# Kernel tuning notes

Hardware: AMD Instinct MI355X
Metric: run time of the kernel (lower is better)

Reference implementation:

```python
import jax, jax.numpy as jnp
import numpy as np

N_HEAD = 16
D_MODEL = 1024
D_K = 64
D_V = 64
LN_EPS = 1e-5


def setup_inputs() -> dict:
    key = jax.random.key(0)
    ks = jax.random.split(key, 12)
    B, S = 4, 1024
    std_qkv = np.sqrt(2.0 / (D_MODEL + D_K)).astype(np.float32)
    inp = {
        "q": jax.random.normal(ks[0], (B, S, D_MODEL), jnp.float32),
        "k": jax.random.normal(ks[1], (B, S, D_MODEL), jnp.float32),
        "v": jax.random.normal(ks[2], (B, S, D_MODEL), jnp.float32),
        "Wq": jax.random.normal(ks[3], (N_HEAD * D_K, D_MODEL), jnp.float32) * std_qkv,
        "bq": jnp.zeros((N_HEAD * D_K,), jnp.float32),
        "Wk": jax.random.normal(ks[4], (N_HEAD * D_K, D_MODEL), jnp.float32) * std_qkv,
        "bk": jnp.zeros((N_HEAD * D_K,), jnp.float32),
        "Wv": jax.random.normal(ks[5], (N_HEAD * D_K, D_MODEL), jnp.float32) * std_qkv,
        "bv": jnp.zeros((N_HEAD * D_K,), jnp.float32),
        "Wfc": jax.random.normal(ks[6], (D_MODEL, N_HEAD * D_V), jnp.float32) * np.sqrt(2.0 / (D_MODEL + N_HEAD * D_V)).astype(np.float32),
        "bfc": jnp.zeros((D_MODEL,), jnp.float32),
        "gamma": jnp.ones((D_MODEL,), jnp.float32),
        "beta": jnp.zeros((D_MODEL,), jnp.float32),
    }
    return inp


def reference(q, k, v, Wq, bq, Wk, bk, Wv, bv, Wfc, bfc, gamma, beta):
    B, S, D = q.shape
    residual = q
    # projections -> [B, S, H, d] -> [B, H, S, d]
    qh = (q @ Wq.T + bq).reshape(B, S, N_HEAD, D_K).transpose(0, 2, 1, 3)
    kh = (k @ Wk.T + bk).reshape(B, S, N_HEAD, D_K).transpose(0, 2, 1, 3)
    vh = (v @ Wv.T + bv).reshape(B, S, N_HEAD, D_V).transpose(0, 2, 1, 3)
    # NOTE: faithful to source -- no 1/sqrt(d_k) scaling (temperature is None)
    scores = jnp.einsum('bhqd,bhkd->bhqk', qh, kh)  # [B, H, S, S]
    attn = jax.nn.softmax(scores, axis=-1)
    out = jnp.einsum('bhqk,bhkd->bhqd', attn, vh)  # [B, H, S, d_v]
    out = out.transpose(0, 2, 1, 3).reshape(B, S, N_HEAD * D_V)
    out = out @ Wfc.T + bfc  # dropout = identity at eval
    x = out + residual
    mu = jnp.mean(x, axis=-1, keepdims=True)
    var = jnp.var(x, axis=-1, keepdims=True)
    y = (x - mu) * jax.lax.rsqrt(var + LN_EPS) * gamma + beta
    # attn returned in source layout: (n_head*batch, S, S)
    attn_flat = attn.transpose(1, 0, 2, 3).reshape(N_HEAD * B, S, S)
    return (y, attn_flat)
```

## Files before the change

### kernel.cpp

```cpp
#include <hip/hip_runtime.h>
#include <stdint.h>

#define B_ 4
#define S_ 1024
#define D_ 1024
#define H_ 16
#define DK_ 64

typedef unsigned short u16;
typedef unsigned int   u32;
typedef short bf16x8 __attribute__((ext_vector_type(8)));
typedef float f32x4  __attribute__((ext_vector_type(4)));

__device__ __forceinline__ u16 f2bf(float x) {
    u32 u = __float_as_uint(x);
    return (u16)((u + 0x7fffu + ((u >> 16) & 1u)) >> 16);
}
__device__ __forceinline__ float bf2f(u16 h) {
    return __uint_as_float(((u32)h) << 16);
}

template <int OMODE>
__global__ __launch_bounds__(256) void gemm_mfma(const float* __restrict__ A,
                                                 const float* __restrict__ W,
                                                 const float* __restrict__ bias,
                                                 float* __restrict__ Cf,
                                                 u16* __restrict__ Chi,
                                                 u16* __restrict__ Clo,
                                                 int M, int N, int K) {
    __shared__ __align__(16) u16 AhS[128][40];
    __shared__ __align__(16) u16 AlS[128][40];
    __shared__ __align__(16) u16 WhS[128][40];
    __shared__ __align__(16) u16 WlS[128][40];

    const int t    = threadIdx.x;
    const int m0   = blockIdx.y * 128;
    const int n0   = blockIdx.x * 128;
    const int srow = t >> 1;
    const int sk   = (t & 1) * 16;
    const int w    = t >> 6;
    const int lane = t & 63;
    const int wr   = w >> 1, wc = w & 1;
    const int fr   = lane & 15;
    const int kg   = lane >> 4;

    const float* Abase = A + (size_t)(m0 + srow) * K + sk;
    const float* Wbase = W + (size_t)(n0 + srow) * K + sk;

    float4 pa[4], pw[4];
#pragma unroll
    for (int i = 0; i < 4; ++i) {
        pa[i] = *(const float4*)(Abase + i * 4);
        pw[i] = *(const float4*)(Wbase + i * 4);
    }

    f32x4 acc[4][4] = {};

    for (int kc = 0; kc < K; kc += 32) {
        u32 hA[8], lA[8], hW[8], lW[8];
#pragma unroll
        for (int i = 0; i < 4; ++i) {
            float xs[4] = {pa[i].x, pa[i].y, pa[i].z, pa[i].w};
            float ys[4] = {pw[i].x, pw[i].y, pw[i].z, pw[i].w};
#pragma unroll
            for (int j = 0; j < 2; ++j) {
                u16 a0 = f2bf(xs[2 * j]), a1 = f2bf(xs[2 * j + 1]);
                hA[i * 2 + j] = (u32)a0 | ((u32)a1 << 16);
                lA[i * 2 + j] = (u32)f2bf(xs[2 * j] - bf2f(a0)) |
                                ((u32)f2bf(xs[2 * j + 1] - bf2f(a1)) << 16);
                u16 w0 = f2bf(ys[2 * j]), w1 = f2bf(ys[2 * j + 1]);
                hW[i * 2 + j] = (u32)w0 | ((u32)w1 << 16);
                lW[i * 2 + j] = (u32)f2bf(ys[2 * j] - bf2f(w0)) |
                                ((u32)f2bf(ys[2 * j + 1] - bf2f(w1)) << 16);
            }
        }
        *(uint4*)&AhS[srow][sk]     = make_uint4(hA[0], hA[1], hA[2], hA[3]);
        *(uint4*)&AhS[srow][sk + 8] = make_uint4(hA[4], hA[5], hA[6], hA[7]);
        *(uint4*)&AlS[srow][sk]     = make_uint4(lA[0], lA[1], lA[2], lA[3]);
        *(uint4*)&AlS[srow][sk + 8] = make_uint4(lA[4], lA[5], lA[6], lA[7]);
        *(uint4*)&WhS[srow][sk]     = make_uint4(hW[0], hW[1], hW[2], hW[3]);
        *(uint4*)&WhS[srow][sk + 8] = make_uint4(hW[4], hW[5], hW[6], hW[7]);
        *(uint4*)&WlS[srow][sk]     = make_uint4(lW[0], lW[1], lW[2], lW[3]);
        *(uint4*)&WlS[srow][sk + 8] = make_uint4(lW[4], lW[5], lW[6], lW[7]);
        __syncthreads();

        if (kc + 32 < K) {
#pragma unroll
            for (int i = 0; i < 4; ++i) {
                pa[i] = *(const float4*)(Abase + kc + 32 + i * 4);
                pw[i] = *(const float4*)(Wbase + kc + 32 + i * 4);
            }
        }

        bf16x8 fah[4], fal[4], fwh[4], fwl[4];
#pragma unroll
        for (int mt = 0; mt < 4; ++mt) {
            fah[mt] = *(const bf16x8*)&AhS[wr * 64 + mt * 16 + fr][kg * 8];
            fal[mt] = *(const bf16x8*)&AlS[wr * 64 + mt * 16 + fr][kg * 8];
        }
#pragma unroll
        for (int nt = 0; nt < 4; ++nt) {
            fwh[nt] = *(const bf16x8*)&WhS[wc * 64 + nt * 16 + fr][kg * 8];
            fwl[nt] = *(const bf16x8*)&WlS[wc * 64 + nt * 16 + fr][kg * 8];
        }
#pragma unroll
        for (int mt = 0; mt < 4; ++mt)
#pragma unroll
            for (int nt = 0; nt < 4; ++nt) {
                acc[mt][nt] = __builtin_amdgcn_mfma_f32_16x16x32_bf16(
                    fah[mt], fwh[nt], acc[mt][nt], 0, 0, 0);
                acc[mt][nt] = __builtin_amdgcn_mfma_f32_16x16x32_bf16(
                    fah[mt], fwl[nt], acc[mt][nt], 0, 0, 0);
                acc[mt][nt] = __builtin_amdgcn_mfma_f32_16x16x32_bf16(
                    fal[mt], fwh[nt], acc[mt][nt], 0, 0, 0);
            }
        __syncthreads();
    }

#pragma unroll
    for (int nt = 0; nt < 4; ++nt) {
        const int n  = n0 + wc * 64 + nt * 16 + fr;
        const float bn = bias[n];
#pragma unroll
        for (int mt = 0; mt < 4; ++mt) {
#pragma unroll
            for (int r = 0; r < 4; ++r) {
                const int m = m0 + wr * 64 + mt * 16 + kg * 4 + r;
                const float v = acc[mt][nt][r] + bn;
                if (OMODE == 0) {
                    Cf[(size_t)m * N + n] = v;
                } else {
                    const int b = m >> 10, s = m & (S_ - 1);
                    const int h = n >> 6, d = n & 63;
                    const size_t off = (((size_t)b * H_ + h) * S_ + s) * DK_ + d;
                    if (OMODE == 2) {
                        Cf[off] = v;
                    } else {
                        const u16 hh = f2bf(v);
                        Chi[off] = hh;
                        Clo[off] = f2bf(v - bf2f(hh));
                    }
                }
            }
        }
    }
}

__global__ __launch_bounds__(256) void scores_mfma(const u16* __restrict__ Qhi,
                                                   const u16* __restrict__ Qlo,
                                                   const u16* __restrict__ Khi,
                                                   const u16* __restrict__ Klo,
                                                   float* __restrict__ Sc) {
    const int bh = blockIdx.z;
    const int b = bh >> 4, h = bh & 15;
    const u16* Qh_g = Qhi + (size_t)bh * S_ * DK_;
    const u16* Ql_g = Qlo + (size_t)bh * S_ * DK_;
    const u16* Kh_g = Khi + (size_t)bh * S_ * DK_;
    const u16* Kl_g = Klo + (size_t)bh * S_ * DK_;
    float* C = Sc + (size_t)(h * B_ + b) * S_ * S_;

    __shared__ __align__(16) u16 AhS[128][40];
    __shared__ __align__(16) u16 AlS[128][40];
    __shared__ __align__(16) u16 WhS[128][40];
    __shared__ __align__(16) u16 WlS[128][40];

    const int t    = threadIdx.x;
    const int m0   = blockIdx.y * 128;
    const int n0   = blockIdx.x * 128;
    const int srow = t >> 1;
    const int sk   = (t & 1) * 16;
    const int w    = t >> 6;
    const int lane = t & 63;
    const int wr   = w >> 1, wc = w & 1;
    const int fr   = lane & 15;
    const int kg   = lane >> 4;

    f32x4 acc[4][4] = {};

    for (int kc = 0; kc < DK_; kc += 32) {
        {
            const size_t qa = (size_t)(m0 + srow) * DK_ + kc + sk;
            const size_t ka = (size_t)(n0 + srow) * DK_ + kc + sk;
            uint4 q0 = *(const uint4*)(Qh_g + qa);
            uint4 q1 = *(const uint4*)(Qh_g + qa + 8);
            uint4 q2 = *(const uint4*)(Ql_g + qa);
            uint4 q3 = *(const uint4*)(Ql_g + qa + 8);
            uint4 k0 = *(const uint4*)(Kh_g + ka);
            uint4 k1 = *(const uint4*)(Kh_g + ka + 8);
            uint4 k2 = *(const uint4*)(Kl_g + ka);
            uint4 k3 = *(const uint4*)(Kl_g + ka + 8);
            *(uint4*)&AhS[srow][sk]     = q0;
            *(uint4*)&AhS[srow][sk + 8] = q1;
            *(uint4*)&AlS[srow][sk]     = q2;
            *(uint4*)&AlS[srow][sk + 8] = q3;
            *(uint4*)&WhS[srow][sk]     = k0;
            *(uint4*)&WhS[srow][sk + 8] = k1;
            *(uint4*)&WlS[srow][sk]     = k2;
            *(uint4*)&WlS[srow][sk + 8] = k3;
        }
        __syncthreads();

        bf16x8 fah[4], fal[4], fwh[4], fwl[4];
#pragma unroll
        for (int mt = 0; mt < 4; ++mt) {
            fah[mt] = *(const bf16x8*)&AhS[wr * 64 + mt * 16 + fr][kg * 8];
            fal[mt] = *(const bf16x8*)&AlS[wr * 64 + mt * 16 + fr][kg * 8];
        }
#pragma unroll
        for (int nt = 0; nt < 4; ++nt) {
            fwh[nt] = *(const bf16x8*)&WhS[wc * 64 + nt * 16 + fr][kg * 8];
            fwl[nt] = *(const bf16x8*)&WlS[wc * 64 + nt * 16 + fr][kg * 8];
        }
#pragma unroll
        for (int mt = 0; mt < 4; ++mt)
#pragma unroll
            for (int nt = 0; nt < 4; ++nt) {
                acc[mt][nt] = __builtin_amdgcn_mfma_f32_16x16x32_bf16(
                    fah[mt], fwh[nt], acc[mt][nt], 0, 0, 0);
                acc[mt][nt] = __builtin_amdgcn_mfma_f32_16x16x32_bf16(
                    fah[mt], fwl[nt], acc[mt][nt], 0, 0, 0);
                acc[mt][nt] = __builtin_amdgcn_mfma_f32_16x16x32_bf16(
                    fal[mt], fwh[nt], acc[mt][nt], 0, 0, 0);
            }
        __syncthreads();
    }

#pragma unroll
    for (int nt = 0; nt < 4; ++nt) {
        const int j = n0 + wc * 64 + nt * 16 + fr;
#pragma unroll
        for (int mt = 0; mt < 4; ++mt) {
#pragma unroll
            for (int r = 0; r < 4; ++r) {
                const int i = m0 + wr * 64 + mt * 16 + kg * 4 + r;
                C[(size_t)i * S_ + j] = acc[mt][nt][r];
            }
        }
    }
}

__global__ __launch_bounds__(256) void softmax_rows(float* __restrict__ attn) {
    const size_t row = blockIdx.x;
    float* p = attn + row * S_;
    const int t = threadIdx.x;

    float4 v = ((const float4*)p)[t];
    float mx = fmaxf(fmaxf(v.x, v.y), fmaxf(v.z, v.w));
#pragma unroll
    for (int o = 32; o > 0; o >>= 1) mx = fmaxf(mx, __shfl_xor(mx, o, 64));

    __shared__ float red[8];
    const int w = t >> 6;
    if ((t & 63) == 0) red[w] = mx;
    __syncthreads();
    mx = fmaxf(fmaxf(red[0], red[1]), fmaxf(red[2], red[3]));

    float4 e;
    e.x = __expf(v.x - mx);
    e.y = __expf(v.y - mx);
    e.z = __expf(v.z - mx);
    e.w = __expf(v.w - mx);
    float s = e.x + e.y + e.z + e.w;
#pragma unroll
    for (int o = 32; o > 0; o >>= 1) s += __shfl_xor(s, o, 64);
    if ((t & 63) == 0) red[4 + w] = s;
    __syncthreads();
    s = red[4] + red[5] + red[6] + red[7];

    const float inv = 1.0f / s;
    e.x *= inv; e.y *= inv; e.z *= inv; e.w *= inv;
    ((float4*)p)[t] = e;
}

__global__ __launch_bounds__(256) void attn_pv(const float* __restrict__ attn,
                                               const float* __restrict__ Vh,
                                               float* __restrict__ ctx) {
    const int bh = blockIdx.y;
    const int b = bh >> 4, h = bh & 15;
    const int i0 = blockIdx.x * 256;
    const int t  = threadIdx.x;
    const int tm = t >> 3;
    const int tn = t & 7;
    const int srow = t >> 2;
    const int scg  = (t & 3) * 4;
    const int vrow = t >> 4;
    const int vcg  = (t & 15) * 4;

    __shared__ float As[16][260];
    __shared__ float Vs[16][68];

    const float* abase = attn + ((size_t)(h * B_ + b) * S_ + i0) * S_;
    const float* vbase = Vh + (size_t)bh * S_ * DK_;

    const float* Ar0 = abase + (size_t)(srow)       * S_ + scg;
    const float* Ar1 = abase + (size_t)(srow + 64)  * S_ + scg;
    const float* Ar2 = abase + (size_t)(srow + 128) * S_ + scg;
    const float* Ar3 = abase + (size_t)(srow + 192) * S_ + scg;
    const float* Vr  = vbase + (size_t)vrow * DK_ + vcg;

    float4 pa0 = *(const float4*)Ar0;
    float4 pa1 = *(const float4*)Ar1;
    float4 pa2 = *(const float4*)Ar2;
    float4 pa3 = *(const float4*)Ar3;
    float4 pv  = *(const float4*)Vr;

    float acc[8][8] = {};

    for (int kc = 0; kc < S_; kc += 16) {
        As[scg + 0][srow]       = pa0.x;
        As[scg + 1][srow]       = pa0.y;
        As[scg + 2][srow]       = pa0.z;
        As[scg + 3][srow]       = pa0.w;
        As[scg + 0][srow + 64]  = pa1.x;
        As[scg + 1][srow + 64]  = pa1.y;
        As[scg + 2][srow + 64]  = pa1.z;
        As[scg + 3][srow + 64]  = pa1.w;
        As[scg + 0][srow + 128] = pa2.x;
        As[scg + 1][srow + 128] = pa2.y;
        As[scg + 2][srow + 128] = pa2.z;
        As[scg + 3][srow + 128] = pa2.w;
        As[scg + 0][srow + 192] = pa3.x;
        As[scg + 1][srow + 192] = pa3.y;
        As[scg + 2][srow + 192] = pa3.z;
        As[scg + 3][srow + 192] = pa3.w;
        *(float4*)&Vs[vrow][vcg] = pv;
        __syncthreads();
        if (kc + 16 < S_) {
            pa0 = *(const float4*)(Ar0 + kc + 16);
            pa1 = *(const float4*)(Ar1 + kc + 16);
            pa2 = *(const float4*)(Ar2 + kc + 16);
            pa3 = *(const float4*)(Ar3 + kc + 16);
            pv  = *(const float4*)(Vr + (size_t)(kc + 16) * DK_);
        }
#pragma unroll
        for (int kk = 0; kk < 16; ++kk) {
            float4 a0 = *(const float4*)&As[kk][tm * 8];
            float4 a1 = *(const float4*)&As[kk][tm * 8 + 4];
            float4 v0 = *(const float4*)&Vs[kk][tn * 4];
            float4 v1 = *(const float4*)&Vs[kk][32 + tn * 4];
            float av[8] = {a0.x, a0.y, a0.z, a0.w, a1.x, a1.y, a1.z, a1.w};
            float vv[8] = {v0.x, v0.y, v0.z, v0.w, v1.x, v1.y, v1.z, v1.w};
#pragma unroll
            for (int i = 0; i < 8; ++i)
#pragma unroll
                for (int j = 0; j < 8; ++j) acc[i][j] += av[i] * vv[j];
        }
        __syncthreads();
    }

#pragma unroll
    for (int i = 0; i < 8; ++i) {
        const int m = i0 + tm * 8 + i;
        float* crow = ctx + ((size_t)b * S_ + m) * D_ + h * DK_;
        *(float4*)(crow + tn * 4) =
            make_float4(acc[i][0], acc[i][1], acc[i][2], acc[i][3]);
        *(float4*)(crow + 32 + tn * 4) =
            make_float4(acc[i][4], acc[i][5], acc[i][6], acc[i][7]);
    }
}

__global__ __launch_bounds__(256) void ln_kernel(const float* __restrict__ X,
                                                 const float* __restrict__ q,
                                                 const float* __restrict__ gamma,
                                                 const float* __restrict__ beta,
                                                 float* __restrict__ y) {
    const int row = blockIdx.x;
    const int t   = threadIdx.x;
    const size_t base = (size_t)row * D_;

    float4 xv = *(const float4*)(X + base + t * 4);
    float4 qv = *(const float4*)(q + base + t * 4);
    const float x0 = xv.x + qv.x, x1 = xv.y + qv.y;
    const float x2 = xv.z + qv.z, x3 = xv.w + qv.w;

    float sum = x0 + x1 + x2 + x3;
    float sq  = x0 * x0 + x1 * x1 + x2 * x2 + x3 * x3;
#pragma unroll
    for (int o = 32; o > 0; o >>= 1) {
        sum += __shfl_xor(sum, o, 64);
        sq  += __shfl_xor(sq, o, 64);
    }
    __shared__ float red[8];
    const int wv = t >> 6;
    if ((t & 63) == 0) { red[wv] = sum; red[4 + wv] = sq; }
    __syncthreads();
    sum = red[0] + red[1] + red[2] + red[3];
    sq  = red[4] + red[5] + red[6] + red[7];

    const float mu  = sum * (1.0f / 1024.0f);
    const float var = sq * (1.0f / 1024.0f) - mu * mu;
    const float rs  = rsqrtf(var + 1e-5f);

    float4 gv = *(const float4*)(gamma + t * 4);
    float4 bv = *(const float4*)(beta + t * 4);
    float4 o;
    o.x = (x0 - mu) * rs * gv.x + bv.x;
    o.y = (x1 - mu) * rs * gv.y + bv.y;
    o.z = (x2 - mu) * rs * gv.z + bv.z;
    o.w = (x3 - mu) * rs * gv.w + bv.w;
    *(float4*)(y + base + t * 4) = o;
}

extern "C" void kernel_launch(void* const* d_in, const int* in_sizes, int n_in,
                              void* d_out, int out_size, void* d_ws, size_t ws_size,
                              hipStream_t stream) {
    const float* q    = (const float*)d_in[0];
    const float* k    = (const float*)d_in[1];
    const float* v    = (const float*)d_in[2];
    const float* Wq   = (const float*)d_in[3];
    const float* bq   = (const float*)d_in[4];
    const float* Wk   = (const float*)d_in[5];
    const float* bk   = (const float*)d_in[6];
    const float* Wv   = (const float*)d_in[7];
    const float* bv   = (const float*)d_in[8];
    const float* Wfc  = (const float*)d_in[9];
    const float* bfc  = (const float*)d_in[10];
    const float* gamma= (const float*)d_in[11];
    const float* beta = (const float*)d_in[12];

    float* y_out    = (float*)d_out;
    float* attn_out = (float*)d_out + (size_t)B_ * S_ * D_;

    float* ws  = (float*)d_ws;
    float* Vh  = ws;
    u16*  Qhi  = (u16*)(ws + 4194304);
    u16*  Qlo  = (u16*)(ws + 6291456);
    u16*  Khi  = (u16*)(ws + 8388608);
    u16*  Klo  = (u16*)(ws + 10485760);
    float* ctx  = ws + 4194304;
    float* xbuf = ws + 8388608;

    const dim3 gg(8, 32), bb(256);
    gemm_mfma<1><<<gg, bb, 0, stream>>>(q, Wq, bq, nullptr, Qhi, Qlo, 4096, 1024, 1024);
    gemm_mfma<1><<<gg, bb, 0, stream>>>(k, Wk, bk, nullptr, Khi, Klo, 4096, 1024, 1024);
    gemm_mfma<2><<<gg, bb, 0, stream>>>(v, Wv, bv, Vh, nullptr, nullptr, 4096, 1024, 1024);

    scores_mfma<<<dim3(8, 8, 64), bb, 0, stream>>>(Qhi, Qlo, Khi, Klo, attn_out);
    softmax_rows<<<dim3(B_ * H_ * S_), bb, 0, stream>>>(attn_out);

    attn_pv<<<dim3(4, 64), bb, 0, stream>>>(attn_out, Vh, ctx);

    gemm_mfma<0><<<gg, bb, 0, stream>>>(ctx, Wfc, bfc, xbuf, nullptr, nullptr, 4096, 1024, 1024);
    ln_kernel<<<4096, 256, 0, stream>>>(xbuf, q, gamma, beta, y_out);
}
```

Before: 809.8 us.

## Fuse scores, softmax and PV into one MFMA attention kernel with bf16 V/ctx

Replaces the separate scores, softmax and fp32 PV kernels with a single kernel. Each block computes a full 32-row strip of scores with split-bf16 MFMA, does the softmax in registers, writes the attention matrix once, and runs P·V on MFMA from bf16 P and a transposed bf16 V. This removes the write-read-write-read round trips of the 256MB attention matrix and the slow scalar-FMA PV loop. The V projection now emits transposed bf16, and the context feeds the output GEMM as bf16 with no low-part correction terms. This lowers precision for P, V and ctx and keeps 128 fp32 accumulators per thread, which may hurt occupancy.

Result: faster. 694.3 us (-14.3%).

```diff
diff --git a/kernel.cpp b/kernel.cpp
--- a/kernel.cpp
+++ b/kernel.cpp
@@ -20,8 +20,8 @@
     return __uint_as_float(((u32)h) << 16);
 }
 
-template <int OMODE>
-__global__ __launch_bounds__(256) void gemm_mfma(const float* __restrict__ A,
+template <int OMODE, int AMODE>
+__global__ __launch_bounds__(256) void gemm_mfma(const void* __restrict__ Ain,
                                                  const float* __restrict__ W,
                                                  const float* __restrict__ bias,
                                                  float* __restrict__ Cf,
@@ -44,59 +44,92 @@
     const int fr   = lane & 15;
     const int kg   = lane >> 4;
 
-    const float* Abase = A + (size_t)(m0 + srow) * K + sk;
+    const float* Af = (const float*)Ain;
+    const u16*   Ab = (const u16*)Ain;
+
     const float* Wbase = W + (size_t)(n0 + srow) * K + sk;
-
-    float4 pa[4], pw[4];
-#pragma unroll
-    for (int i = 0; i < 4; ++i) {
-        pa[i] = *(const float4*)(Abase + i * 4);
-        pw[i] = *(const float4*)(Wbase + i * 4);
+    float4 pw[4];
+#pragma unroll
+    for (int i = 0; i < 4; ++i) pw[i] = *(const float4*)(Wbase + i * 4);
+
+    float4 pa[4];
+    uint4  ua[2];
+    if constexpr (AMODE == 0) {
+        const float* Abase = Af + (size_t)(m0 + srow) * K + sk;
+#pragma unroll
+        for (int i = 0; i < 4; ++i) pa[i] = *(const float4*)(Abase + i * 4);
+    } else {
+        const u16* Abase = Ab + (size_t)(m0 + srow) * K + sk;
+        ua[0] = *(const uint4*)(Abase);
+        ua[1] = *(const uint4*)(Abase + 8);
     }
 
     f32x4 acc[4][4] = {};
 
     for (int kc = 0; kc < K; kc += 32) {
-        u32 hA[8], lA[8], hW[8], lW[8];
-#pragma unroll
-        for (int i = 0; i < 4; ++i) {
-            float xs[4] = {pa[i].x, pa[i].y, pa[i].z, pa[i].w};
-            float ys[4] = {pw[i].x, pw[i].y, pw[i].z, pw[i].w};
-#pragma unroll
-            for (int j = 0; j < 2; ++j) {
-                u16 a0 = f2bf(xs[2 * j]), a1 = f2bf(xs[2 * j + 1]);
-                hA[i * 2 + j] = (u32)a0 | ((u32)a1 << 16);
-                lA[i * 2 + j] = (u32)f2bf(xs[2 * j] - bf2f(a0)) |
-                                ((u32)f2bf(xs[2 * j + 1] - bf2f(a1)) << 16);
-                u16 w0 = f2bf(ys[2 * j]), w1 = f2bf(ys[2 * j + 1]);
-                hW[i * 2 + j] = (u32)w0 | ((u32)w1 << 16);
-                lW[i * 2 + j] = (u32)f2bf(ys[2 * j] - bf2f(w0)) |
-                                ((u32)f2bf(ys[2 * j + 1] - bf2f(w1)) << 16);
-            }
-        }
-        *(uint4*)&AhS[srow][sk]     = make_uint4(hA[0], hA[1], hA[2], hA[3]);
-        *(uint4*)&AhS[srow][sk + 8] = make_uint4(hA[4], hA[5], hA[6], hA[7]);
-        *(uint4*)&AlS[srow][sk]     = make_uint4(lA[0], lA[1], lA[2], lA[3]);
-        *(uint4*)&AlS[srow][sk + 8] = make_uint4(lA[4], lA[5], lA[6], lA[7]);
-        *(uint4*)&WhS[srow][sk]     = make_uint4(hW[0], hW[1], hW[2], hW[3]);
-        *(uint4*)&WhS[srow][sk + 8] = make_uint4(hW[4], hW[5], hW[6], hW[7]);
-        *(uint4*)&WlS[srow][sk]     = make_uint4(lW[0], lW[1], lW[2], lW[3]);
-        *(uint4*)&WlS[srow][sk + 8] = make_uint4(lW[4], lW[5], lW[6], lW[7]);
+        if constexpr (AMODE == 0) {
+            u32 hA[8], lA[8];
+#pragma unroll
+            for (int i = 0; i < 4; ++i) {
+                float xs[4] = {pa[i].x, pa[i].y, pa[i].z, pa[i].w};
+#pragma unroll
+                for (int j = 0; j < 2; ++j) {
+                    u16 a0 = f2bf(xs[2 * j]), a1 = f2bf(xs[2 * j + 1]);
+                    hA[i * 2 + j] = (u32)a0 | ((u32)a1 << 16);
+                    lA[i * 2 + j] = (u32)f2bf(xs[2 * j] - bf2f(a0)) |
+                                    ((u32)f2bf(xs[2 * j + 1] - bf2f(a1)) << 16);
+                }
+            }
+            *(uint4*)&AhS[srow][sk]     = make_uint4(hA[0], hA[1], hA[2], hA[3]);
+            *(uint4*)&AhS[srow][sk + 8] = make_uint4(hA[4], hA[5], hA[6], hA[7]);
+            *(uint4*)&AlS[srow][sk]     = make_uint4(lA[0], lA[1], lA[2], lA[3]);
+            *(uint4*)&AlS[srow][sk + 8] = make_uint4(lA[4], lA[5], lA[6], lA[7]);
+        } else {
+            *(uint4*)&AhS[srow][sk]     = ua[0];
+            *(uint4*)&AhS[srow][sk + 8] = ua[1];
+        }
+        {
+            u32 hW[8], lW[8];
+#pragma unroll
+            for (int i = 0; i < 4; ++i) {
+                float ys[4] = {pw[i].x, pw[i].y, pw[i].z, pw[i].w};
+#pragma unroll
+                for (int j = 0; j < 2; ++j) {
+                    u16 w0 = f2bf(ys[2 * j]), w1 = f2bf(ys[2 * j + 1]);
+                    hW[i * 2 + j] = (u32)w0 | ((u32)w1 << 16);
+                    lW[i * 2 + j] = (u32)f2bf(ys[2 * j] - bf2f(w0)) |
+                                    ((u32)f2bf(ys[2 * j + 1] - bf2f(w1)) << 16);
+                }
+            }
+            *(uint4*)&WhS[srow][sk]     = make_uint4(hW[0], hW[1], hW[2], hW[3]);
+            *(uint4*)&WhS[srow][sk + 8] = make_uint4(hW[4], hW[5], hW[6], hW[7]);
+            *(uint4*)&WlS[srow][sk]     = make_uint4(lW[0], lW[1], lW[2], lW[3]);
+            *(uint4*)&WlS[srow][sk + 8] = make_uint4(lW[4], lW[5], lW[6], lW[7]);
+        }
         __syncthreads();
 
         if (kc + 32 < K) {
-#pragma unroll
-            for (int i = 0; i < 4; ++i) {
-                pa[i] = *(const float4*)(Abase + kc + 32 + i * 4);
+            if constexpr (AMODE == 0) {
+                const float* Abase = Af + (size_t)(m0 + srow) * K + sk;
+#pragma unroll
+                for (int i = 0; i < 4; ++i)
+                    pa[i] = *(const float4*)(Abase + kc + 32 + i * 4);
+            } else {
+                const u16* Abase = Ab + (size_t)(m0 + srow) * K + sk;
+                ua[0] = *(const uint4*)(Abase + kc + 32);
+                ua[1] = *(const uint4*)(Abase + kc + 32 + 8);
+            }
+#pragma unroll
+            for (int i = 0; i < 4; ++i)
                 pw[i] = *(const float4*)(Wbase + kc + 32 + i * 4);
-            }
         }
 
         bf16x8 fah[4], fal[4], fwh[4], fwl[4];
 #pragma unroll
         for (int mt = 0; mt < 4; ++mt) {
             fah[mt] = *(const bf16x8*)&AhS[wr * 64 + mt * 16 + fr][kg * 8];
-            fal[mt] = *(const bf16x8*)&AlS[wr * 64 + mt * 16 + fr][kg * 8];
+            if constexpr (AMODE == 0)
+                fal[mt] = *(const bf16x8*)&AlS[wr * 64 + mt * 16 + fr][kg * 8];
         }
 #pragma unroll
         for (int nt = 0; nt < 4; ++nt) {
@@ -111,8 +144,9 @@
                     fah[mt], fwh[nt], acc[mt][nt], 0, 0, 0);
                 acc[mt][nt] = __builtin_amdgcn_mfma_f32_16x16x32_bf16(
                     fah[mt], fwl[nt], acc[mt][nt], 0, 0, 0);
-                acc[mt][nt] = __builtin_amdgcn_mfma_f32_16x16x32_bf16(
-                    fal[mt], fwh[nt], acc[mt][nt], 0, 0, 0);
+                if constexpr (AMODE == 0)
+                    acc[mt][nt] = __builtin_amdgcn_mfma_f32_16x16x32_bf16(
+                        fal[mt], fwh[nt], acc[mt][nt], 0, 0, 0);
             }
         __syncthreads();
     }
@@ -132,13 +166,13 @@
                 } else {
                     const int b = m >> 10, s = m & (S_ - 1);
                     const int h = n >> 6, d = n & 63;
-                    const size_t off = (((size_t)b * H_ + h) * S_ + s) * DK_ + d;
-                    if (OMODE == 2) {
-                        Cf[off] = v;
-                    } else {
+                    if (OMODE == 1) {
+                        const size_t off = (((size_t)b * H_ + h) * S_ + s) * DK_ + d;
                         const u16 hh = f2bf(v);
                         Chi[off] = hh;
                         Clo[off] = f2bf(v - bf2f(hh));
+                    } else {
+                        Chi[(((size_t)b * H_ + h) * DK_ + d) * S_ + s] = f2bf(v);
                     }
                 }
             }
@@ -146,217 +180,194 @@
     }
 }
 
-__global__ __launch_bounds__(256) void scores_mfma(const u16* __restrict__ Qhi,
-                                                   const u16* __restrict__ Qlo,
-                                                   const u16* __restrict__ Khi,
-                                                   const u16* __restrict__ Klo,
-                                                   float* __restrict__ Sc) {
-    const int bh = blockIdx.z;
-    const int b = bh >> 4, h = bh & 15;
-    const u16* Qh_g = Qhi + (size_t)bh * S_ * DK_;
-    const u16* Ql_g = Qlo + (size_t)bh * S_ * DK_;
-    const u16* Kh_g = Khi + (size_t)bh * S_ * DK_;
-    const u16* Kl_g = Klo + (size_t)bh * S_ * DK_;
-    float* C = Sc + (size_t)(h * B_ + b) * S_ * S_;
-
-    __shared__ __align__(16) u16 AhS[128][40];
-    __shared__ __align__(16) u16 AlS[128][40];
-    __shared__ __align__(16) u16 WhS[128][40];
-    __shared__ __align__(16) u16 WlS[128][40];
-
-    const int t    = threadIdx.x;
-    const int m0   = blockIdx.y * 128;
-    const int n0   = blockIdx.x * 128;
-    const int srow = t >> 1;
-    const int sk   = (t & 1) * 16;
-    const int w    = t >> 6;
+__global__ __launch_bounds__(256) void fused_attn(const u16* __restrict__ Qhi,
+                                                  const u16* __restrict__ Qlo,
+                                                  const u16* __restrict__ Khi,
+                                                  const u16* __restrict__ Klo,
+                                                  const u16* __restrict__ VT,
+                                                  float* __restrict__ attn,
+                                                  u16* __restrict__ ctx) {
+    const int bh = blockIdx.y;
+    const int b  = bh >> 4, h = bh & 15;
+    const int i0 = blockIdx.x * 32;
+    const int t  = threadIdx.x;
+    const int w  = t >> 6;
     const int lane = t & 63;
-    const int wr   = w >> 1, wc = w & 1;
-    const int fr   = lane & 15;
-    const int kg   = lane >> 4;
-
-    f32x4 acc[4][4] = {};
-
-    for (int kc = 0; kc < DK_; kc += 32) {
-        {
-            const size_t qa = (size_t)(m0 + srow) * DK_ + kc + sk;
-            const size_t ka = (size_t)(n0 + srow) * DK_ + kc + sk;
-            uint4 q0 = *(const uint4*)(Qh_g + qa);
-            uint4 q1 = *(const uint4*)(Qh_g + qa + 8);
-            uint4 q2 = *(const uint4*)(Ql_g + qa);
-            uint4 q3 = *(const uint4*)(Ql_g + qa + 8);
-            uint4 k0 = *(const uint4*)(Kh_g + ka);
-            uint4 k1 = *(const uint4*)(Kh_g + ka + 8);
-            uint4 k2 = *(const uint4*)(Kl_g + ka);
-            uint4 k3 = *(const uint4*)(Kl_g + ka + 8);
-            *(uint4*)&AhS[srow][sk]     = q0;
-            *(uint4*)&AhS[srow][sk + 8] = q1;
-            *(uint4*)&AlS[srow][sk]     = q2;
-            *(uint4*)&AlS[srow][sk + 8] = q3;
-            *(uint4*)&WhS[srow][sk]     = k0;
-            *(uint4*)&WhS[srow][sk + 8] = k1;
-            *(uint4*)&WlS[srow][sk]     = k2;
-            *(uint4*)&WlS[srow][sk + 8] = k3;
-        }
-        __syncthreads();
-
-        bf16x8 fah[4], fal[4], fwh[4], fwl[4];
-#pragma unroll
-        for (int mt = 0; mt < 4; ++mt) {
-            fah[mt] = *(const bf16x8*)&AhS[wr * 64 + mt * 16 + fr][kg * 8];
-            fal[mt] = *(const bf16x8*)&AlS[wr * 64 + mt * 16 + fr][kg * 8];
-        }
-#pragma unroll
-        for (int nt = 0; nt < 4; ++nt) {
-            fwh[nt] = *(const bf16x8*)&WhS[wc * 64 + nt * 16 + fr][kg * 8];
-            fwl[nt] = *(const bf16x8*)&WlS[wc * 64 + nt * 16 + fr][kg * 8];
-        }
-#pragma unroll
-        for (int mt = 0; mt < 4; ++mt)
-#pragma unroll
-            for (int nt = 0; nt < 4; ++nt) {
-                acc[mt][nt] = __builtin_amdgcn_mfma_f32_16x16x32_bf16(
-                    fah[mt], fwh[nt], acc[mt][nt], 0, 0, 0);
-                acc[mt][nt] = __builtin_amdgcn_mfma_f32_16x16x32_bf16(
-                    fah[mt], fwl[nt], acc[mt][nt], 0, 0, 0);
-                acc[mt][nt] = __builtin_amdgcn_mfma_f32_16x16x32_bf16(
-                    fal[mt], fwh[nt], acc[mt][nt], 0, 0, 0);
-            }
-        __syncthreads();
-    }
-
-#pragma unroll
-    for (int nt = 0; nt < 4; ++nt) {
-        const int j = n0 + wc * 64 + nt * 16 + fr;
-#pragma unroll
-        for (int mt = 0; mt < 4; ++mt) {
+    const int c  = lane & 15;
+    const int q  = lane >> 4;
+
+    __shared__ __align__(16) u16 smem[2 * 128 * 64];
+    u16* KhiL = smem;
+    u16* KloL = smem + 128 * 64;
+    u16* Pl   = smem;
+    u16* VTl  = smem + 32 * 128;
+    __shared__ float redS[4][32];
+
+    bf16x8 qh[2][2], ql[2][2];
+#pragma unroll
+    for (int mt = 0; mt < 2; ++mt)
+#pragma unroll
+        for (int kf = 0; kf < 2; ++kf) {
+            const size_t off = ((size_t)bh * S_ + i0 + mt * 16 + c) * DK_ + kf * 32 + q * 8;
+            qh[mt][kf] = *(const bf16x8*)(Qhi + off);
+            ql[mt][kf] = *(const bf16x8*)(Qlo + off);
+        }
+
+    f32x4 acc[2][16] = {};
+
+#pragma unroll
+    for (int ch = 0; ch < 8; ++ch) {
+        __syncthreads();
+#pragma unroll
+        for (int u = 0; u < 4; ++u) {
+            const int unit = t * 4 + u;
+            const int j = unit >> 3, k16 = unit & 7;
+            const int dstb = j * 128 + ((k16 * 16) ^ ((j & 7) << 4));
+            const size_t src = ((size_t)bh * S_ + ch * 128 + j) * DK_ + k16 * 8;
+            *(uint4*)((char*)KhiL + dstb) = *(const uint4*)(Khi + src);
+            *(uint4*)((char*)KloL + dstb) = *(const uint4*)(Klo + src);
+        }
+        __syncthreads();
+#pragma unroll
+        for (int ct = 0; ct < 2; ++ct) {
+            const int j = w * 32 + ct * 16 + c;
+#pragma unroll
+            for (int kf = 0; kf < 2; ++kf) {
+                const int byt = j * 128 + ((kf * 64 + q * 16) ^ ((j & 7) << 4));
+                bf16x8 kh = *(const bf16x8*)((char*)KhiL + byt);
+                bf16x8 kl = *(const bf16x8*)((char*)KloL + byt);
+#pragma unroll
+                for (int mt = 0; mt < 2; ++mt) {
+                    acc[mt][ch * 2 + ct] = __builtin_amdgcn_mfma_f32_16x16x32_bf16(
+                        qh[mt][kf], kh, acc[mt][ch * 2 + ct], 0, 0, 0);
+                    acc[mt][ch * 2 + ct] = __builtin_amdgcn_mfma_f32_16x16x32_bf16(
+                        ql[mt][kf], kh, acc[mt][ch * 2 + ct], 0, 0, 0);
+                    acc[mt][ch * 2 + ct] = __builtin_amdgcn_mfma_f32_16x16x32_bf16(
+                        qh[mt][kf], kl, acc[mt][ch * 2 + ct], 0, 0, 0);
+                }
+            }
+        }
+    }
+
+    float mx[2][4];
+#pragma unroll
+    for (int mt = 0; mt < 2; ++mt)
+#pragma unroll
+        for (int r = 0; r < 4; ++r) {
+            float m = -1e30f;
+#pragma unroll
+            for (int ci = 0; ci < 16; ++ci) m = fmaxf(m, acc[mt][ci][r]);
+#pragma unroll
+            for (int o = 1; o < 16; o <<= 1) m = fmaxf(m, __shfl_xor(m, o, 64));
+            mx[mt][r] = m;
+        }
+    if (c == 0) {
+#pragma unroll
+        for (int mt = 0; mt < 2; ++mt)
+#pragma unroll
+            for (int r = 0; r < 4; ++r) redS[w][mt * 16 + q * 4 + r] = mx[mt][r];
+    }
+    __syncthreads();
+#pragma unroll
+    for (int mt = 0; mt < 2; ++mt)
+#pragma unroll
+        for (int r = 0; r < 4; ++r) {
+            const int row = mt * 16 + q * 4 + r;
+            mx[mt][r] = fmaxf(fmaxf(redS[0][row], redS[1][row]),
+                              fmaxf(redS[2][row], redS[3][row]));
+        }
+    float sm[2][4] = {};
+#pragma unroll
+    for (int mt = 0; mt < 2; ++mt)
+#pragma unroll
+        for (int ci = 0; ci < 16; ++ci)
 #pragma unroll
             for (int r = 0; r < 4; ++r) {
-                const int i = m0 + wr * 64 + mt * 16 + kg * 4 + r;
-                C[(size_t)i * S_ + j] = acc[mt][nt][r];
-            }
-        }
-    }
-}
-
-__global__ __launch_bounds__(256) void softmax_rows(float* __restrict__ attn) {
-    const size_t row = blockIdx.x;
-    float* p = attn + row * S_;
-    const int t = threadIdx.x;
-
-    float4 v = ((const float4*)p)[t];
-    float mx = fmaxf(fmaxf(v.x, v.y), fmaxf(v.z, v.w));
-#pragma unroll
-    for (int o = 32; o > 0; o >>= 1) mx = fmaxf(mx, __shfl_xor(mx, o, 64));
-
-    __shared__ float red[8];
-    const int w = t >> 6;
-    if ((t & 63) == 0) red[w] = mx;
+                const float e = __expf(acc[mt][ci][r] - mx[mt][r]);
+                acc[mt][ci][r] = e;
+                sm[mt][r] += e;
+            }
+#pragma unroll
+    for (int mt = 0; mt < 2; ++mt)
+#pragma unroll
+        for (int r = 0; r < 4; ++r)
+#pragma unroll
+            for (int o = 1; o < 16; o <<= 1) sm[mt][r] += __shfl_xor(sm[mt][r], o, 64);
     __syncthreads();
-    mx = fmaxf(fmaxf(red[0], red[1]), fmaxf(red[2], red[3]));
-
-    float4 e;
-    e.x = __expf(v.x - mx);
-    e.y = __expf(v.y - mx);
-    e.z = __expf(v.z - mx);
-    e.w = __expf(v.w - mx);
-    float s = e.x + e.y + e.z + e.w;
-#pragma unroll
-    for (int o = 32; o > 0; o >>= 1) s += __shfl_xor(s, o, 64);
-    if ((t & 63) == 0) red[4 + w] = s;
+    if (c == 0) {
+#pragma unroll
+        for (int mt = 0; mt < 2; ++mt)
+#pragma unroll
+            for (int r = 0; r < 4; ++r) redS[w][mt * 16 + q * 4 + r] = sm[mt][r];
+    }
     __syncthreads();
-    s = red[4] + red[5] + red[6] + red[7];
-
-    const float inv = 1.0f / s;
-    e.x *= inv; e.y *= inv; e.z *= inv; e.w *= inv;
-    ((float4*)p)[t] = e;
-}
-
-__global__ __launch_bounds__(256) void attn_pv(const float* __restrict__ attn,
-                                               const float* __restrict__ Vh,
-                                               float* __restrict__ ctx) {
-    const int bh = blockIdx.y;
-    const int b = bh >> 4, h = bh & 15;
-    const int i0 = blockIdx.x * 256;
-    const int t  = threadIdx.x;
-    const int tm = t >> 3;
-    const int tn = t & 7;
-    const int srow = t >> 2;
-    const int scg  = (t & 3) * 4;
-    const int vrow = t >> 4;
-    const int vcg  = (t & 15) * 4;
-
-    __shared__ float As[16][260];
-    __shared__ float Vs[16][68];
-
-    const float* abase = attn + ((size_t)(h * B_ + b) * S_ + i0) * S_;
-    const float* vbase = Vh + (size_t)bh * S_ * DK_;
-
-    const float* Ar0 = abase + (size_t)(srow)       * S_ + scg;
-    const float* Ar1 = abase + (size_t)(srow + 64)  * S_ + scg;
-    const float* Ar2 = abase + (size_t)(srow + 128) * S_ + scg;
-    const float* Ar3 = abase + (size_t)(srow + 192) * S_ + scg;
-    const float* Vr  = vbase + (size_t)vrow * DK_ + vcg;
-
-    float4 pa0 = *(const float4*)Ar0;
-    float4 pa1 = *(const float4*)Ar1;
-    float4 pa2 = *(const float4*)Ar2;
-    float4 pa3 = *(const float4*)Ar3;
-    float4 pv  = *(const float4*)Vr;
-
-    float acc[8][8] = {};
-
-    for (int kc = 0; kc < S_; kc += 16) {
-        As[scg + 0][srow]       = pa0.x;
-        As[scg + 1][srow]       = pa0.y;
-        As[scg + 2][srow]       = pa0.z;
-        As[scg + 3][srow]       = pa0.w;
-        As[scg + 0][srow + 64]  = pa1.x;
-        As[scg + 1][srow + 64]  = pa1.y;
-        As[scg + 2][srow + 64]  = pa1.z;
-        As[scg + 3][srow + 64]  = pa1.w;
-        As[scg + 0][srow + 128] = pa2.x;
-        As[scg + 1][srow + 128] = pa2.y;
-        As[scg + 2][srow + 128] = pa2.z;
-        As[scg + 3][srow + 128] = pa2.w;
-        As[scg + 0][srow + 192] = pa3.x;
-        As[scg + 1][srow + 192] = pa3.y;
-        As[scg + 2][srow + 192] = pa3.z;
-        As[scg + 3][srow + 192] = pa3.w;
-        *(float4*)&Vs[vrow][vcg] = pv;
-        __syncthreads();
-        if (kc + 16 < S_) {
-            pa0 = *(const float4*)(Ar0 + kc + 16);
-            pa1 = *(const float4*)(Ar1 + kc + 16);
-            pa2 = *(const float4*)(Ar2 + kc + 16);
-            pa3 = *(const float4*)(Ar3 + kc + 16);
-            pv  = *(const float4*)(Vr + (size_t)(kc + 16) * DK_);
-        }
-#pragma unroll
-        for (int kk = 0; kk < 16; ++kk) {
-            float4 a0 = *(const float4*)&As[kk][tm * 8];
-            float4 a1 = *(const float4*)&As[kk][tm * 8 + 4];
-            float4 v0 = *(const float4*)&Vs[kk][tn * 4];
-            float4 v1 = *(const float4*)&Vs[kk][32 + tn * 4];
-            float av[8] = {a0.x, a0.y, a0.z, a0.w, a1.x, a1.y, a1.z, a1.w};
-            float vv[8] = {v0.x, v0.y, v0.z, v0.w, v1.x, v1.y, v1.z, v1.w};
-#pragma unroll
-            for (int i = 0; i < 8; ++i)
-#pragma unroll
-                for (int j = 0; j < 8; ++j) acc[i][j] += av[i] * vv[j];
-        }
-        __syncthreads();
-    }
-
-#pragma unroll
-    for (int i = 0; i < 8; ++i) {
-        const int m = i0 + tm * 8 + i;
-        float* crow = ctx + ((size_t)b * S_ + m) * D_ + h * DK_;
-        *(float4*)(crow + tn * 4) =
-            make_float4(acc[i][0], acc[i][1], acc[i][2], acc[i][3]);
-        *(float4*)(crow + 32 + tn * 4) =
-            make_float4(acc[i][4], acc[i][5], acc[i][6], acc[i][7]);
-    }
+    float inv[2][4];
+#pragma unroll
+    for (int mt = 0; mt < 2; ++mt)
+#pragma unroll
+        for (int r = 0; r < 4; ++r) {
+            const int row = mt * 16 + q * 4 + r;
+            inv[mt][r] = 1.0f / (redS[0][row] + redS[1][row] + redS[2][row] + redS[3][row]);
+        }
+    float* dst = attn + ((size_t)(h * B_ + b) * S_ + i0) * S_;
+#pragma unroll
+    for (int mt = 0; mt < 2; ++mt)
+#pragma unroll
+        for (int ci = 0; ci < 16; ++ci)
+#pragma unroll
+            for (int r = 0; r < 4; ++r) {
+                const float p = acc[mt][ci][r] * inv[mt][r];
+                acc[mt][ci][r] = p;
+                const int row = mt * 16 + q * 4 + r;
+                const int col = (ci >> 1) * 128 + w * 32 + (ci & 1) * 16 + c;
+                dst[(size_t)row * S_ + col] = p;
+            }
+
+    f32x4 c2[2] = {};
+#pragma unroll
+    for (int ch = 0; ch < 8; ++ch) {
+        __syncthreads();
+#pragma unroll
+        for (int mt = 0; mt < 2; ++mt)
+#pragma unroll
+            for (int ct = 0; ct < 2; ++ct)
+#pragma unroll
+                for (int r = 0; r < 4; ++r) {
+                    const int row = mt * 16 + q * 4 + r;
+                    const int col = w * 32 + ct * 16 + c;
+                    const int byt = row * 256 + ((col * 2) ^ ((row & 7) << 4));
+                    *(u16*)((char*)Pl + byt) = f2bf(acc[mt][ch * 2 + ct][r]);
+                }
+#pragma unroll
+        for (int u = 0; u < 4; ++u) {
+            const int unit = t * 4 + u;
+            const int d = unit >> 4, s16 = unit & 15;
+            const int byt = d * 256 + ((s16 * 16) ^ ((d & 7) << 4));
+            *(uint4*)((char*)VTl + byt) =
+                *(const uint4*)(VT + ((size_t)bh * DK_ + d) * S_ + ch * 128 + s16 * 8);
+        }
+        __syncthreads();
+#pragma unroll
+        for (int kf = 0; kf < 4; ++kf) {
+            const int dloc = w * 16 + c;
+            const int vb_byt = dloc * 256 + ((kf * 64 + q * 16) ^ ((c & 7) << 4));
+            bf16x8 vb = *(const bf16x8*)((char*)VTl + vb_byt);
+#pragma unroll
+            for (int mt = 0; mt < 2; ++mt) {
+                const int pr = mt * 16 + c;
+                const int pa_byt = pr * 256 + ((kf * 64 + q * 16) ^ ((c & 7) << 4));
+                bf16x8 pa = *(const bf16x8*)((char*)Pl + pa_byt);
+                c2[mt] = __builtin_amdgcn_mfma_f32_16x16x32_bf16(pa, vb, c2[mt], 0, 0, 0);
+            }
+        }
+    }
+#pragma unroll
+    for (int mt = 0; mt < 2; ++mt)
+#pragma unroll
+        for (int r = 0; r < 4; ++r) {
+            const int s = i0 + mt * 16 + q * 4 + r;
+            ctx[((size_t)b * S_ + s) * D_ + h * DK_ + w * 16 + c] = f2bf(c2[mt][r]);
+        }
 }
 
 __global__ __launch_bounds__(256) void ln_kernel(const float* __restrict__ X,
@@ -421,25 +432,22 @@
     float* y_out    = (float*)d_out;
     float* attn_out = (float*)d_out + (size_t)B_ * S_ * D_;
 
-    float* ws  = (float*)d_ws;
-    float* Vh  = ws;
-    u16*  Qhi  = (u16*)(ws + 4194304);
-    u16*  Qlo  = (u16*)(ws + 6291456);
-    u16*  Khi  = (u16*)(ws + 8388608);
-    u16*  Klo  = (u16*)(ws + 10485760);
-    float* ctx  = ws + 4194304;
-    float* xbuf = ws + 8388608;
+    float* ws   = (float*)d_ws;
+    u16*  Qhi   = (u16*)(ws);
+    u16*  Qlo   = (u16*)(ws + 2097152);
+    u16*  Khi   = (u16*)(ws + 4194304);
+    u16*  Klo   = (u16*)(ws + 6291456);
+    u16*  VTb   = (u16*)(ws + 8388608);
+    u16*  ctxb  = (u16*)(ws + 10485760);
+    float* xbuf = ws;
 
     const dim3 gg(8, 32), bb(256);
-    gemm_mfma<1><<<gg, bb, 0, stream>>>(q, Wq, bq, nullptr, Qhi, Qlo, 4096, 1024, 1024);
-    gemm_mfma<1><<<gg, bb, 0, stream>>>(k, Wk, bk, nullptr, Khi, Klo, 4096, 1024, 1024);
-    gemm_mfma<2><<<gg, bb, 0, stream>>>(v, Wv, bv, Vh, nullptr, nullptr, 4096, 1024, 1024);
-
-    scores_mfma<<<dim3(8, 8, 64), bb, 0, stream>>>(Qhi, Qlo, Khi, Klo, attn_out);
-    softmax_rows<<<dim3(B_ * H_ * S_), bb, 0, stream>>>(attn_out);
-
-    attn_pv<<<dim3(4, 64), bb, 0, stream>>>(attn_out, Vh, ctx);
-
-    gemm_mfma<0><<<gg, bb, 0, stream>>>(ctx, Wfc, bfc, xbuf, nullptr, nullptr, 4096, 1024, 1024);
+    gemm_mfma<1, 0><<<gg, bb, 0, stream>>>(q, Wq, bq, nullptr, Qhi, Qlo, 4096, 1024, 1024);
+    gemm_mfma<1, 0><<<gg, bb, 0, stream>>>(k, Wk, bk, nullptr, Khi, Klo, 4096, 1024, 1024);
+    gemm_mfma<2, 0><<<gg, bb, 0, stream>>>(v, Wv, bv, nullptr, VTb, nullptr, 4096, 1024, 1024);
+
+    fused_attn<<<dim3(32, 64), bb, 0, stream>>>(Qhi, Qlo, Khi, Klo, VTb, attn_out, ctxb);
+
+    gemm_mfma<0, 1><<<gg, bb, 0, stream>>>(ctxb, Wfc, bfc, xbuf, nullptr, nullptr, 4096, 1024, 1024);
     ln_kernel<<<4096, 256, 0, stream>>>(xbuf, q, gamma, beta, y_out);
 }
```
